# Kernel tuning notes

Measured on AMD Instinct MI355X. Metric: run time of the kernel, lower is better.

## Reference

```python
import jax, jax.numpy as jnp
import numpy as np

B = 4096
HIST = 50
VOCAB = 100000
PAD_IDX = 179
EMB_DIM = 64           # sparse_dim_after_embedding
DENSE = 256            # dense_feature_number
PROJ_IN = 768          # emb_feature_dim_before_project
PROJ_HID = 256
PROJ_OUT = 64          # emb_feature_dim
BOT = (512, 64)        # bottom_mlp_dims
ALL_DIM = EMB_DIM + BOT[1] + PROJ_OUT        # 192
OUT_DIM = ALL_DIM * (ALL_DIM + 1) // 2 + BOT[1]  # 18592
TOP = (1024, 512)      # top_mlp_dims
BN_EPS = 1e-5

# precomputed upper-triangular (incl. diagonal) indices, row-major like torch mask extract
_TRIU_R, _TRIU_C = np.triu_indices(ALL_DIM)


def setup_inputs() -> dict:
    key = jax.random.key(0)
    ks = jax.random.split(key, 20)
    s = 0.02
    emb_table = jax.random.normal(ks[0], (VOCAB, EMB_DIM), jnp.float32) * s
    emb_table = emb_table.at[PAD_IDX].set(0.0)  # padding_idx=179
    return {
        "x_sparse": jax.random.randint(ks[1], (B, HIST), 0, VOCAB),
        "x_dense": jax.random.normal(ks[2], (B, DENSE), jnp.float32),
        "x_embed_before_projection": jax.random.normal(ks[3], (B, PROJ_IN), jnp.float32),
        "emb_table": emb_table,
        "pw1": jax.random.normal(ks[4], (PROJ_IN, PROJ_HID), jnp.float32) * s,
        "pb1": jnp.zeros((PROJ_HID,), jnp.float32),
        "pw2": jax.random.normal(ks[5], (PROJ_HID, PROJ_OUT), jnp.float32) * s,
        "pb2": jnp.zeros((PROJ_OUT,), jnp.float32),
        "bn_gamma": jnp.ones((PROJ_OUT,), jnp.float32),
        "bn_beta": jnp.zeros((PROJ_OUT,), jnp.float32),
        "bw1": jax.random.normal(ks[6], (DENSE, BOT[0]), jnp.float32) * s,
        "bb1": jnp.zeros((BOT[0],), jnp.float32),
        "bw2": jax.random.normal(ks[7], (BOT[0], BOT[1]), jnp.float32) * s,
        "bb2": jnp.zeros((BOT[1],), jnp.float32),
        "tw1": jax.random.normal(ks[8], (OUT_DIM, TOP[0]), jnp.float32) * s,
        "tb1": jnp.zeros((TOP[0],), jnp.float32),
        "tw2": jax.random.normal(ks[9], (TOP[0], TOP[1]), jnp.float32) * s,
        "tb2": jnp.zeros((TOP[1],), jnp.float32),
        "tw3": jax.random.normal(ks[10], (TOP[1], 1), jnp.float32) * s,
        "tb3": jnp.zeros((1,), jnp.float32),
    }


def reference(x_sparse, x_dense, x_embed_before_projection, emb_table,
              pw1, pb1, pw2, pb2, bn_gamma, bn_beta,
              bw1, bb1, bw2, bb2, tw1, tb1, tw2, tb2, tw3, tb3):
    # embedding-sum over history: [B, HIST, EMB_DIM] -> [B, EMB_DIM]
    embed_x = jnp.sum(emb_table[x_sparse], axis=1)

    # ContrastiveNet: Linear -> ReLU -> Linear -> BatchNorm1d (batch stats, training fwd)
    h = jax.nn.relu(x_embed_before_projection @ pw1 + pb1)
    z = h @ pw2 + pb2
    mu = jnp.mean(z, axis=0)
    var = jnp.var(z, axis=0)  # biased variance, as torch BN uses for normalization
    x_embed = bn_gamma * (z - mu) * jax.lax.rsqrt(var + BN_EPS) + bn_beta

    # bottom MLP (dropout = identity at inference)
    bottom = jax.nn.relu(jax.nn.relu(x_dense @ bw1 + bb1) @ bw2 + bb2)

    concat_first = jnp.concatenate([bottom, x_embed, embed_x], axis=-1)  # [B, 192]

    # pairwise dot-product interaction; pack upper triangle incl. diagonal
    dot = jnp.einsum('bi,bj->bij', concat_first, concat_first)  # [B, 192, 192]
    interaction = dot[:, _TRIU_R, _TRIU_C]  # [B, 192*193/2]

    concat_second = jnp.concatenate([interaction, bottom], axis=-1)  # [B, OUT_DIM]

    t = jax.nn.relu(concat_second @ tw1 + tb1)
    t = jax.nn.relu(t @ tw2 + tb2)
    output = jax.nn.sigmoid(t @ tw3 + tb3)  # [B, 1]
    # squeeze(-1).squeeze().unsqueeze(1) -> [B, 1]
    output = output.reshape(-1, 1)
    return output, x_embed
```

## Files before the change

kernel.cpp:

```cpp
#include <hip/hip_runtime.h>
#include <hip/hip_bf16.h>
#include <cstdint>
#include <cstddef>

typedef __bf16 bf16;
typedef unsigned char u8;
typedef unsigned short u16;
typedef __bf16 v8bf  __attribute__((ext_vector_type(8)));
typedef float  f32x4 __attribute__((ext_vector_type(4)));
typedef float  f32x16 __attribute__((ext_vector_type(16)));
typedef int    i32x4 __attribute__((ext_vector_type(4)));
typedef int    i32x2 __attribute__((ext_vector_type(2)));
typedef int    v8i32 __attribute__((ext_vector_type(8)));

__device__ __forceinline__ void async16(void* lds, const void* g) {
  __builtin_amdgcn_global_load_lds(
      (const __attribute__((address_space(1))) unsigned int*)g,
      (__attribute__((address_space(3))) unsigned int*)lds, 16, 0, 0);
}


__device__ __forceinline__ void pairs_dev(u16* __restrict__ pairs, float* __restrict__ stats) {
  int r = threadIdx.x;
  if (r < 128) stats[r] = 0.f;
  if (r < 192) {
    int off = 192 * r - (r * (r - 1)) / 2;
    for (int c = r; c < 192; ++c) pairs[off + c - r] = (u16)((r << 8) | c);
  } else if (r == 192) {
    for (int j = 0; j < 64; ++j) pairs[18528 + j] = (u16)((j << 8) | 192);
  } else if (r == 193) {
    for (int j = 18592; j < 18624; ++j) pairs[j] = (u16)((192 << 8) | 192);
  }
}

__device__ __forceinline__ void packA_dev(const float* __restrict__ A,
                                          bf16* __restrict__ Ap, int K,
                                          int bx, int by) {
  const int t = threadIdx.x;
  const int KT = K >> 5;
  const size_t tile = ((size_t)bx * KT + by) * (64 * 32);
  const int c = t;
  const int mm = c >> 2, koct = (c & 3) * 8;
  const float* src = A + (size_t)(bx * 64 + mm) * K + by * 32 + koct;
  f32x4 f0 = *(const f32x4*)src;
  f32x4 f1 = *(const f32x4*)(src + 4);
  __align__(16) bf16 h[8];
  h[0]=(bf16)f0[0]; h[1]=(bf16)f0[1]; h[2]=(bf16)f0[2]; h[3]=(bf16)f0[3];
  h[4]=(bf16)f1[0]; h[5]=(bf16)f1[1]; h[6]=(bf16)f1[2]; h[7]=(bf16)f1[3];
  *(i32x4*)(Ap + tile + (size_t)c * 8) = *(const i32x4*)h;
}

__device__ __forceinline__ void packB_dev(const float* __restrict__ B,
                                          bf16* __restrict__ Bp, int K, int N,
                                          int bx, int by,
                                          float* __restrict__ sLB) {
  const int BNp = 64, LS = 66;
  const int t = threadIdx.x;
  const int KT = K >> 5;
  for (int idx = t; idx < 32 * BNp; idx += 256) {
    const int kk = idx >> 6, nn = idx & 63;
    sLB[kk * LS + nn] = B[(size_t)(by * 32 + kk) * N + bx * BNp + nn];
  }
  __syncthreads();
  const size_t tile = ((size_t)bx * KT + by) * ((size_t)BNp * 32);
  for (int c = t; c < BNp * 4; c += 256) {
    const int nn = c >> 2, koct = (c & 3) * 8;
    __align__(16) bf16 h[8];
#pragma unroll
    for (int j = 0; j < 8; ++j) h[j] = (bf16)sLB[(koct + j) * LS + nn];
    *(i32x4*)(Bp + tile + (size_t)c * 8) = *(const i32x4*)h;
  }
}

__device__ __forceinline__ void packTw1_dev(const float* __restrict__ tw1,
                                            u8* __restrict__ Bp, int nt, int kw) {
  const int t = threadIdx.x;
  const int n4 = t & 31, k8 = t >> 5;
  const int kbase = kw * 64 + k8 * 8;
  const int nbase = nt * 128 + n4 * 4;
  f32x4 v[8];
#pragma unroll
  for (int j = 0; j < 8; ++j) {
    const int gk = kbase + j;
    if (gk < 18592) {
      v[j] = *(const f32x4*)(tw1 + (size_t)gk * 1024 + nbase);
      v[j] *= 32.f;
    } else {
      v[j] = f32x4{0.f, 0.f, 0.f, 0.f};
    }
  }
  u8* tile = Bp + ((size_t)nt * 291 + kw) * 8192;
#pragma unroll
  for (int c = 0; c < 4; ++c) {
    int r0 = __builtin_amdgcn_cvt_pk_fp8_f32(v[0][c], v[1][c], 0, false);
    r0 = __builtin_amdgcn_cvt_pk_fp8_f32(v[2][c], v[3][c], r0, true);
    int r1 = __builtin_amdgcn_cvt_pk_fp8_f32(v[4][c], v[5][c], 0, false);
    r1 = __builtin_amdgcn_cvt_pk_fp8_f32(v[6][c], v[7][c], r1, true);
    i32x2 d; d[0] = r0; d[1] = r1;
    *(i32x2*)(tile + (n4 * 4 + c) * 64 + k8 * 8) = d;
  }
}

__global__ __launch_bounds__(256) void prologue_kernel(
    const float* __restrict__ xep, const float* __restrict__ xd,
    const float* __restrict__ pw1, const float* __restrict__ pw2,
    const float* __restrict__ bw1, const float* __restrict__ bw2,
    const float* __restrict__ tw1, const float* __restrict__ tw2,
    bf16* Xp, bf16* Xd, bf16* Bpw1, bf16* Bpw2, bf16* Bbw1, bf16* Bbw2,
    u8* Btw1, bf16* Btw2, u16* pairs, float* stats) {
  __shared__ float sLB[32 * 66];
  int i = blockIdx.x;
  if (i < 2328) { packTw1_dev(tw1, Btw1, i & 7, i >> 3); return; }
  i -= 2328;
  if (i < 1536) { packA_dev(xep, Xp, 768, i & 63, i >> 6); return; }
  i -= 1536;
  if (i < 512)  { packA_dev(xd, Xd, 256, i & 63, i >> 6); return; }
  i -= 512;
  if (i < 96)   { packB_dev(pw1, Bpw1, 768, 256, i & 3, i >> 2, sLB); return; }
  i -= 96;
  if (i < 8)    { packB_dev(pw2, Bpw2, 256, 64, 0, i, sLB); return; }
  i -= 8;
  if (i < 64)   { packB_dev(bw1, Bbw1, 256, 512, i & 7, i >> 3, sLB); return; }
  i -= 64;
  if (i < 16)   { packB_dev(bw2, Bbw2, 512, 64, 0, i, sLB); return; }
  i -= 16;
  if (i < 256)  { packB_dev(tw2, Btw2, 1024, 512, i & 7, i >> 3, sLB); return; }
  i -= 256;
  if (i == 0) pairs_dev(pairs, stats);
}

__device__ __forceinline__ void embed8_dev(const int* __restrict__ xs,
                                           const float* __restrict__ emb,
                                           float* __restrict__ cf, int blk) {
  const int wid = threadIdx.x >> 6, lane = threadIdx.x & 63;
#pragma unroll
  for (int s = 0; s < 2; ++s) {
    const int b = blk * 8 + s * 4 + wid;
    const int* row = xs + (size_t)b * 50;
    float acc = 0.f;
#pragma unroll 10
    for (int h = 0; h < 50; ++h) {
      int idx = row[h];
      acc += emb[(size_t)idx * 64 + lane];
    }
    cf[(size_t)b * 193 + 128 + lane] = acc;
  }
}

template <int BM, int BN, int MF, int NF>
__device__ __forceinline__ void gemm_body(
    const bf16* __restrict__ Ap, const bf16* __restrict__ Bp,
    const float* __restrict__ bias,
    float* __restrict__ outF, int ldF,
    bf16* __restrict__ outP, int ktN, int bmsh,
    int KT, int M0, int relu_flag, int bx, int by,
    bf16* sA, bf16* sB, float* statsAcc) {
  const int t = threadIdx.x;
  const int wid = t >> 6, lane = t & 63;
  const int wm = (wid >> 1) * (MF * 16);
  const int wn = (wid & 1) * (NF * 16);
  const int r16 = lane & 15, q = lane >> 4;

  f32x4 acc[MF][NF];
#pragma unroll
  for (int i = 0; i < MF; ++i)
#pragma unroll
    for (int j = 0; j < NF; ++j) acc[i][j] = f32x4{0.f, 0.f, 0.f, 0.f};

  const bf16* aBase = Ap + (size_t)bx * KT * (BM * 32);
  const bf16* bBase = Bp + (size_t)by * KT * (BN * 32);
  constexpr int A_CH = BM * 4;
  constexpr int B_CH = BN * 4;

  for (int kt = 0; kt < KT; ++kt) {
    const bf16* ag = aBase + (size_t)kt * (BM * 32);
    const bf16* bg = bBase + (size_t)kt * (BN * 32);
#pragma unroll
    for (int c = t; c < A_CH; c += 256) {
      const int row = c >> 2, qs = c & 3, qg = (qs - (row >> 1)) & 3;
      async16(sA + c * 8, ag + row * 32 + qg * 8);
    }
#pragma unroll
    for (int c = t; c < B_CH; c += 256) {
      const int row = c >> 2, qs = c & 3, qg = (qs - (row >> 1)) & 3;
      async16(sB + c * 8, bg + row * 32 + qg * 8);
    }
    __syncthreads();
    v8bf af[MF], bfr[NF];
#pragma unroll
    for (int i = 0; i < MF; ++i) {
      const int row = wm + i * 16 + r16;
      af[i] = *(const v8bf*)(sA + row * 32 + (((q + (row >> 1)) & 3) * 8));
    }
#pragma unroll
    for (int j = 0; j < NF; ++j) {
      const int row = wn + j * 16 + r16;
      bfr[j] = *(const v8bf*)(sB + row * 32 + (((q + (row >> 1)) & 3) * 8));
    }
#pragma unroll
    for (int i = 0; i < MF; ++i)
#pragma unroll
      for (int j = 0; j < NF; ++j)
        acc[i][j] = __builtin_amdgcn_mfma_f32_16x16x32_bf16(af[i], bfr[j], acc[i][j], 0, 0, 0);
    __syncthreads();
  }

  float cs[NF], cs2[NF];
#pragma unroll
  for (int j = 0; j < NF; ++j) { cs[j] = 0.f; cs2[j] = 0.f; }

#pragma unroll
  for (int j = 0; j < NF; ++j) {
    const int gn = by * BN + wn + j * 16 + r16;
    const float bv = bias[gn];
#pragma unroll
    for (int i = 0; i < MF; ++i) {
      const int gm0 = M0 + bx * BM + wm + i * 16 + q * 4;
#pragma unroll
      for (int r = 0; r < 4; ++r) {
        float v = acc[i][j][r] + bv;
        if (relu_flag) v = fmaxf(v, 0.f);
        if (statsAcc) { cs[j] += v; cs2[j] += v * v; }
        const int gm = gm0 + r;
        if (outF) outF[(size_t)gm * ldF + gn] = v;
        if (outP) {
          const int mt = gm >> bmsh, mm = gm & ((1 << bmsh) - 1);
          outP[(((size_t)mt * ktN + (gn >> 5)) << (bmsh + 5)) + ((size_t)mm << 5) + (gn & 31)] = (bf16)v;
        }
      }
    }
  }

  if (statsAcc) {
#pragma unroll
    for (int j = 0; j < NF; ++j) {
      float a = cs[j], b2 = cs2[j];
      a += __shfl_xor(a, 16, 64);  a += __shfl_xor(a, 32, 64);
      b2 += __shfl_xor(b2, 16, 64); b2 += __shfl_xor(b2, 32, 64);
      if (q == 0) {
        const int gn = by * BN + wn + j * 16 + r16;
        atomicAdd(&statsAcc[gn], a);
        atomicAdd(&statsAcc[64 + gn], b2);
      }
    }
  }
}

template <int BM, int BN, int MF, int NF>
__global__ __launch_bounds__(256, 2) void gemm_kernel(
    const bf16* __restrict__ Ap, const bf16* __restrict__ Bp,
    const float* __restrict__ bias,
    float* __restrict__ outF, int ldF,
    bf16* __restrict__ outP, int ktN, int bmsh,
    int KT, int M0, int relu_flag) {
  __shared__ __align__(16) bf16 sA[BM * 32];
  __shared__ __align__(16) bf16 sB[BN * 32];
  gemm_body<BM, BN, MF, NF>(Ap, Bp, bias, outF, ldF, outP, ktN, bmsh,
                            KT, M0, relu_flag, blockIdx.x, blockIdx.y, sA, sB, nullptr);
}

template <int BM, int BN, int MF, int NF>
__global__ __launch_bounds__(256, 2) void gemm_dual_kernel(
    const bf16* Ap0, const bf16* Bp0, const float* bias0,
    float* outF0, int ldF0, bf16* outP0, int ktN0, int bmsh0, int KT0, int relu0, int gy0,
    float* statsAcc0,
    const bf16* Ap1, const bf16* Bp1, const float* bias1,
    float* outF1, int ldF1, bf16* outP1, int ktN1, int bmsh1, int KT1, int relu1, int gy1,
    const int* xs, const float* emb, float* cf) {
  __shared__ __align__(16) bf16 sA[BM * 32];
  __shared__ __align__(16) bf16 sB[BN * 32];
  if (blockIdx.z == 0) {
    if ((int)blockIdx.y >= gy0) return;
    gemm_body<BM, BN, MF, NF>(Ap0, Bp0, bias0, outF0, ldF0, outP0, ktN0, bmsh0,
                              KT0, 0, relu0, blockIdx.x, blockIdx.y, sA, sB, statsAcc0);
  } else if (blockIdx.z == 1) {
    if ((int)blockIdx.y >= gy1) return;
    gemm_body<BM, BN, MF, NF>(Ap1, Bp1, bias1, outF1, ldF1, outP1, ktN1, bmsh1,
                              KT1, 0, relu1, blockIdx.x, blockIdx.y, sA, sB, nullptr);
  } else {
    embed8_dev(xs, emb, cf, blockIdx.y * 64 + blockIdx.x);
  }
}

template <int S>
__global__ __launch_bounds__(256, 4) void gemm_splitk_mx(
    const u8* __restrict__ Ap, const u8* __restrict__ Bp,
    bf16* __restrict__ part, int Mchunk) {
  __shared__ __align__(16) u8 sAB[4][8192];
  const int t = threadIdx.x;
  const int bx = blockIdx.x, by = blockIdx.y, bz = blockIdx.z;
  const int lane = t & 63, wid = t >> 6;
  const int wm = (wid >> 1) * 64, wn = (wid & 1) * 64;
  const int l31 = lane & 31, khalf = lane >> 5;
  const int kw0 = (291 * bz) / S, kw1 = (291 * (bz + 1)) / S;

  const int r1 = t >> 2;
  const int g1 = r1 * 64 + ((((t & 3) - (r1 >> 1)) & 3) << 4);
  const int r2 = (t + 256) >> 2;
  const int g2 = r2 * 64 + (((((t + 256) & 3) - (r2 >> 1)) & 3) << 4);
  u8* lA = &sAB[0][0] + t * 16;
  u8* lB = &sAB[2][0] + t * 16;

  const u8* fa0[2]; const u8* fa1[2]; const u8* fb0[2]; const u8* fb1[2];
#pragma unroll
  for (int i = 0; i < 2; ++i) {
    const int ra = wm + i * 32 + l31;
    const int qa = (khalf * 2 + (ra >> 1)) & 3;
    fa0[i] = &sAB[0][0] + ra * 64 + qa * 16;
    fa1[i] = &sAB[0][0] + ra * 64 + (((qa + 1) & 3) << 4);
    const int rb = wn + i * 32 + l31;
    const int qb = (khalf * 2 + (rb >> 1)) & 3;
    fb0[i] = &sAB[2][0] + rb * 64 + qb * 16;
    fb1[i] = &sAB[2][0] + rb * 64 + (((qb + 1) & 3) << 4);
  }

  f32x16 acc[2][2];
#pragma unroll
  for (int i = 0; i < 2; ++i)
#pragma unroll
    for (int j = 0; j < 2; ++j)
#pragma unroll
      for (int r = 0; r < 16; ++r) acc[i][j][r] = 0.f;

  const u8* agp = Ap + ((size_t)bx * 291 + kw0) * 8192;
  const u8* bgp = Bp + ((size_t)by * 291 + kw0) * 8192;

  auto compute = [&](int off) {
    v8i32 av[2], bv[2];
#pragma unroll
    for (int i = 0; i < 2; ++i) {
      union { i32x4 h[2]; v8i32 v; } ua;
      ua.h[0] = *(const i32x4*)(fa0[i] + off);
      ua.h[1] = *(const i32x4*)(fa1[i] + off);
      av[i] = ua.v;
      union { i32x4 h[2]; v8i32 v; } ub;
      ub.h[0] = *(const i32x4*)(fb0[i] + off);
      ub.h[1] = *(const i32x4*)(fb1[i] + off);
      bv[i] = ub.v;
    }
#pragma unroll
    for (int i = 0; i < 2; ++i)
#pragma unroll
      for (int j = 0; j < 2; ++j)
        acc[i][j] = __builtin_amdgcn_mfma_scale_f32_32x32x64_f8f6f4(
            av[i], bv[j], acc[i][j], 0, 0,
            0, 0x7F7F7F7F,
            0, 0x7A7A7A7A);
  };

  const int nw = kw1 - kw0;
  int w = 0;
  for (; w + 2 <= nw; w += 2) {
    async16(lA, agp + g1);         async16(lA + 4096, agp + g2);
    async16(lB, bgp + g1);         async16(lB + 4096, bgp + g2);
    async16(lA + 8192, agp + 8192 + g1); async16(lA + 12288, agp + 8192 + g2);
    async16(lB + 8192, bgp + 8192 + g1); async16(lB + 12288, bgp + 8192 + g2);
    agp += 16384; bgp += 16384;
    __syncthreads();
    compute(0);
    compute(8192);
    __syncthreads();
  }
  if (w < nw) {
    async16(lA, agp + g1); async16(lA + 4096, agp + g2);
    async16(lB, bgp + g1); async16(lB + 4096, bgp + g2);
    __syncthreads();
    compute(0);
    __syncthreads();
  }

  bf16* pBase = part + (size_t)bz * Mchunk * 1024;
#pragma unroll
  for (int i = 0; i < 2; ++i)
#pragma unroll
    for (int j = 0; j < 2; ++j) {
      const int gn = by * 128 + wn + j * 32 + l31;
#pragma unroll
      for (int r = 0; r < 16; ++r) {
        const int gm = bx * 128 + wm + i * 32 + (r & 3) + 8 * (r >> 2) + 4 * khalf;
        pBase[(size_t)gm * 1024 + gn] = (bf16)acc[i][j][r];
      }
    }
}

__global__ __launch_bounds__(256) void reducek_kernel(const bf16* __restrict__ part,
                                                      const float* __restrict__ bias,
                                                      bf16* __restrict__ t1,
                                                      int S, int Mchunk, int M0) {
  const int idx = blockIdx.x * 256 + threadIdx.x;
  const int gm = idx >> 7;
  const int gn8 = (idx & 127) * 8;
  float v[8] = {0.f, 0.f, 0.f, 0.f, 0.f, 0.f, 0.f, 0.f};
  for (int s = 0; s < S; ++s) {
    v8bf p = *(const v8bf*)(part + ((size_t)s * Mchunk + gm) * 1024 + gn8);
#pragma unroll
    for (int r = 0; r < 8; ++r) v[r] += (float)p[r];
  }
  const f32x4 b0 = *(const f32x4*)(bias + gn8);
  const f32x4 b1 = *(const f32x4*)(bias + gn8 + 4);
  __align__(16) bf16 h[8];
#pragma unroll
  for (int r = 0; r < 4; ++r) h[r] = (bf16)fmaxf(v[r] + b0[r], 0.f);
#pragma unroll
  for (int r = 0; r < 4; ++r) h[4 + r] = (bf16)fmaxf(v[4 + r] + b1[r], 0.f);
  const int G = M0 + gm;
  const int mt = G >> 6, mm = G & 63, kt = gn8 >> 5;
  *(i32x4*)(t1 + (((size_t)mt * 32 + kt) << 11) + (mm << 5) + (gn8 & 31)) = *(const i32x4*)h;
}

__global__ __launch_bounds__(256, 2) void agen_kernel(const float* __restrict__ cf,
                                                      const float* __restrict__ z,
                                                      const float* __restrict__ gsum,
                                                      const float* __restrict__ gamma,
                                                      const float* __restrict__ beta,
                                                      const u16* __restrict__ pairs,
                                                      u8* __restrict__ Ap,
                                                      float* __restrict__ dout,
                                                      int rowBase) {
  __shared__ float sCF[64 * 193];
  __shared__ float sMu[64], sRstd[64];
  const int t = threadIdx.x;
  const int gRow0 = rowBase + blockIdx.x * 64;
  for (int idx = t; idx < 64 * 64; idx += 256) {
    const int r = idx >> 6, c = idx & 63;
    sCF[r * 193 + c] = cf[(size_t)(gRow0 + r) * 193 + c];
  }
  for (int idx = t; idx < 64 * 64; idx += 256) {
    const int r = idx >> 6, c = idx & 63;
    sCF[r * 193 + 128 + c] = cf[(size_t)(gRow0 + r) * 193 + 128 + c];
  }
  if (t < 64) {
    const float mu = gsum[t] * (1.f / 4096.f);
    const float var = gsum[64 + t] * (1.f / 4096.f) - mu * mu;
    sMu[t] = mu;
    sRstd[t] = rsqrtf(var + 1e-5f);
    sCF[t * 193 + 192] = 1.f;
  }
  __syncthreads();
  for (int idx = t; idx < 64 * 64; idx += 256) {
    const int r = idx >> 6, c = idx & 63;
    const float xe = gamma[c] * (z[(size_t)(gRow0 + r) * 64 + c] - sMu[c]) * sRstd[c] + beta[c];
    sCF[r * 193 + 64 + c] = xe;
    if (blockIdx.y == 0) dout[4096 + (size_t)(gRow0 + r) * 64 + c] = xe;
  }
  __syncthreads();

  const int kw0 = (291 * blockIdx.y) / 8;
  const int kw1 = (291 * (blockIdx.y + 1)) / 8;
  const int row = t >> 2, kq = t & 3;
  const int mt = blockIdx.x >> 1;
  const int mrow = (blockIdx.x & 1) * 64 + row;
  const float* myrow = sCF + row * 193;
  for (int kw = kw0; kw < kw1; ++kw) {
    const int kb = kw * 64 + kq * 16;
    i32x4 d;
    if (kb >= 18592) {
      d = i32x4{0, 0, 0, 0};
    } else {
      union { i32x4 v4[2]; u16 u[16]; } P;
      P.v4[0] = *(const i32x4*)(pairs + kb);
      P.v4[1] = *(const i32x4*)(pairs + kb + 8);
#pragma unroll
      for (int g = 0; g < 4; ++g) {
        float p[4];
#pragma unroll
        for (int j = 0; j < 4; ++j) {
          const u16 pr = P.u[g * 4 + j];
          p[j] = myrow[pr >> 8] * myrow[pr & 255];
        }
        int r = __builtin_amdgcn_cvt_pk_fp8_f32(p[0], p[1], 0, false);
        r = __builtin_amdgcn_cvt_pk_fp8_f32(p[2], p[3], r, true);
        d[g] = r;
      }
    }
    *(i32x4*)(Ap + (((size_t)mt * 291 + kw) * 128 + mrow) * 64 + kq * 16) = d;
  }
}

__global__ __launch_bounds__(256) void topdot_kernel(const bf16* __restrict__ t2p,
                                                     const float* __restrict__ w,
                                                     const float* __restrict__ b3,
                                                     float* __restrict__ dout) {
  const int wid = threadIdx.x >> 6, lane = threadIdx.x & 63;
  const int b = blockIdx.x * 4 + wid;
  const size_t addr = ((((size_t)(b >> 6) * 16) + (lane >> 2)) << 11) +
                      ((size_t)(b & 63) << 5) + (lane & 3) * 8;
  v8bf p = *(const v8bf*)(t2p + addr);
  const float* wv = w + lane * 8;
  float s = 0.f;
#pragma unroll
  for (int r = 0; r < 8; ++r) s += (float)p[r] * wv[r];
  for (int m = 32; m > 0; m >>= 1) s += __shfl_xor(s, m, 64);
  if (lane == 0) dout[b] = 1.f / (1.f + __expf(-(s + b3[0])));
}

extern "C" void kernel_launch(void* const* d_in, const int* in_sizes, int n_in,
                              void* d_out, int out_size, void* d_ws, size_t ws_size,
                              hipStream_t stream) {
  const int*   xs   = (const int*)  d_in[0];
  const float* xd   = (const float*)d_in[1];
  const float* xep  = (const float*)d_in[2];
  const float* emb  = (const float*)d_in[3];
  const float* pw1  = (const float*)d_in[4];
  const float* pb1  = (const float*)d_in[5];
  const float* pw2  = (const float*)d_in[6];
  const float* pb2  = (const float*)d_in[7];
  const float* gmma = (const float*)d_in[8];
  const float* beta = (const float*)d_in[9];
  const float* bw1  = (const float*)d_in[10];
  const float* bb1  = (const float*)d_in[11];
  const float* bw2  = (const float*)d_in[12];
  const float* bb2  = (const float*)d_in[13];
  const float* tw1  = (const float*)d_in[14];
  const float* tb1  = (const float*)d_in[15];
  const float* tw2  = (const float*)d_in[16];
  const float* tb2  = (const float*)d_in[17];
  const float* tw3  = (const float*)d_in[18];
  const float* tb3  = (const float*)d_in[19];
  float* out = (float*)d_out;

  uint8_t* base = (uint8_t*)d_ws;
  size_t off = 0;
  auto alloc = [&](size_t b) {
    void* p = base + off;
    off = (off + b + 511) & ~((size_t)511);
    return p;
  };
  u16*  pairs = (u16*) alloc((size_t)18624 * 2);
  bf16* Xp    = (bf16*)alloc((size_t)4096 * 768 * 2);
  bf16* Xd    = (bf16*)alloc((size_t)4096 * 256 * 2);
  bf16* Bpw1  = (bf16*)alloc((size_t)768 * 256 * 2);
  bf16* Bpw2  = (bf16*)alloc((size_t)256 * 64 * 2);
  bf16* Bbw1  = (bf16*)alloc((size_t)256 * 512 * 2);
  bf16* Bbw2  = (bf16*)alloc((size_t)512 * 64 * 2);
  u8*   Btw1  = (u8*)  alloc((size_t)8 * 291 * 8192);
  bf16* Btw2  = (bf16*)alloc((size_t)1024 * 512 * 2);
  bf16* hbuf  = (bf16*)alloc((size_t)4096 * 256 * 2);
  float* z    = (float*)alloc((size_t)4096 * 64 * 4);
  float* stats= (float*)alloc((size_t)128 * 4);
  bf16* b0    = (bf16*)alloc((size_t)4096 * 512 * 2);
  float* cf   = (float*)alloc((size_t)4096 * 193 * 4);
  bf16* t1    = (bf16*)alloc((size_t)4096 * 1024 * 2);
  bf16* t2p   = (bf16*)alloc((size_t)4096 * 512 * 2);
  size_t fixedEnd = off;

  int chunk = 512, S = 8;
  {
    const int candC[5] = {4096, 2048, 2048, 1024, 512};
    const int candS[5] = {4, 8, 4, 8, 8};
    for (int i = 0; i < 5; ++i) {
      size_t need = fixedEnd + (size_t)candC[i] * 18624 + 1024 +
                    (size_t)candS[i] * candC[i] * 1024 * 2 + 1024;
      if (need <= ws_size) { chunk = candC[i]; S = candS[i]; break; }
    }
  }
  u8*   ApBig = (u8*)  alloc((size_t)chunk * 18624);
  bf16* partK = (bf16*)alloc((size_t)S * chunk * 1024 * 2);

  prologue_kernel<<<4817, 256, 0, stream>>>(
      xep, xd, pw1, pw2, bw1, bw2, tw1, tw2,
      Xp, Xd, Bpw1, Bpw2, Bbw1, Bbw2, Btw1, Btw2, pairs, stats);

  gemm_dual_kernel<64, 64, 2, 2><<<dim3(64, 8, 3), 256, 0, stream>>>(
      Xp, Bpw1, pb1, nullptr, 0, hbuf, 8, 6, 24, 1, 4, nullptr,
      Xd, Bbw1, bb1, nullptr, 0, b0, 16, 6, 8, 1, 8,
      xs, emb, cf);
  gemm_dual_kernel<64, 64, 2, 2><<<dim3(64, 1, 2), 256, 0, stream>>>(
      hbuf, Bpw2, pb2, z, 64, nullptr, 0, 0, 8, 0, 1, stats,
      b0, Bbw2, bb2, cf, 193, nullptr, 0, 0, 16, 1, 1,
      nullptr, nullptr, nullptr);

  for (int c0 = 0; c0 < 4096; c0 += chunk) {
    agen_kernel<<<dim3(chunk / 64, 8), 256, 0, stream>>>(
        cf, z, stats, gmma, beta, pairs, ApBig, out, c0);
    if (S == 4)
      gemm_splitk_mx<4><<<dim3(chunk / 128, 8, 4), 256, 0, stream>>>(
          ApBig, Btw1, partK, chunk);
    else
      gemm_splitk_mx<8><<<dim3(chunk / 128, 8, 8), 256, 0, stream>>>(
          ApBig, Btw1, partK, chunk);
    reducek_kernel<<<chunk / 2, 256, 0, stream>>>(partK, tb1, t1, S, chunk, c0);
  }

  gemm_kernel<64, 64, 2, 2><<<dim3(64, 8), 256, 0, stream>>>(
      t1, Btw2, tb2, nullptr, 0, t2p, 16, 6, 32, 0, 1);
  topdot_kernel<<<1024, 256, 0, stream>>>(t2p, tw3, tb3, out);
}
```

Baseline: 349.1 us.

## Double-buffer FP8 GEMM K-loop with async LDS prefetch and waitcnt

Replaces the load-two-chunks-then-compute loop with a ping-pong double buffer. The loads for the next K chunk are issued before computing the current one, and s_waitcnt vmcnt(4) waits only for the current chunk. The MFMA section is wrapped in s_setprio raises. The aim is to hide global-to-LDS latency behind compute, at the cost of a barrier per chunk rather than per two chunks and reliance on manual vmcnt accounting.

```diff
diff --git a/kernel.cpp b/kernel.cpp
--- a/kernel.cpp
+++ b/kernel.cpp
@@ -349,24 +349,28 @@
   };
 
   const int nw = kw1 - kw0;
-  int w = 0;
-  for (; w + 2 <= nw; w += 2) {
-    async16(lA, agp + g1);         async16(lA + 4096, agp + g2);
-    async16(lB, bgp + g1);         async16(lB + 4096, bgp + g2);
-    async16(lA + 8192, agp + 8192 + g1); async16(lA + 12288, agp + 8192 + g2);
-    async16(lB + 8192, bgp + 8192 + g1); async16(lB + 12288, bgp + 8192 + g2);
-    agp += 16384; bgp += 16384;
-    __syncthreads();
-    compute(0);
-    compute(8192);
-    __syncthreads();
-  }
-  if (w < nw) {
-    async16(lA, agp + g1); async16(lA + 4096, agp + g2);
-    async16(lB, bgp + g1); async16(lB + 4096, bgp + g2);
-    __syncthreads();
-    compute(0);
-    __syncthreads();
+
+  async16(lA, agp + g1);  async16(lA + 4096, agp + g2);
+  async16(lB, bgp + g1);  async16(lB + 4096, bgp + g2);
+
+  for (int w = 0; w < nw; ++w) {
+    const int cur = (w & 1) * 8192;
+    const int nxt = 8192 - cur;
+    if (w + 1 < nw) {
+      const u8* ag = agp + (size_t)(w + 1) * 8192;
+      const u8* bg = bgp + (size_t)(w + 1) * 8192;
+      async16(lA + nxt, ag + g1);  async16(lA + nxt + 4096, ag + g2);
+      async16(lB + nxt, bg + g1);  async16(lB + nxt + 4096, bg + g2);
+      asm volatile("s_waitcnt vmcnt(4)" ::: "memory");
+    } else {
+      asm volatile("s_waitcnt vmcnt(0)" ::: "memory");
+    }
+    __builtin_amdgcn_s_barrier();
+    __builtin_amdgcn_sched_barrier(0);
+    __builtin_amdgcn_s_setprio(1);
+    compute(cur);
+    __builtin_amdgcn_s_setprio(0);
+    __builtin_amdgcn_s_barrier();
   }
 
   bf16* pBase = part + (size_t)bz * Mchunk * 1024;
```

After: 354.0 us. Within noise of the previous version (+1.4%).
